# Kernel optimization log

Hardware: AMD Instinct MI355X
Metric: run time of the kernel (lower is better)

The kernel has to match this reference:

```python
import jax, jax.numpy as jnp
import numpy as np

TEMPERATURE = 0.07
EPS = 1e-12  # F.normalize eps


def setup_inputs() -> dict:
    key = jax.random.key(0)
    k1, k2, k3 = jax.random.split(key, 3)
    B, D, N_CLASSES = 4096, 256, 1000
    return {
        "z_i": jax.random.normal(k1, (B, D), dtype=jnp.float32),
        "z_j": jax.random.normal(k2, (B, D), dtype=jnp.float32),
        "labels": jax.random.randint(k3, (B,), 0, N_CLASSES, dtype=jnp.int64),
    }


def _l2_normalize(x):
    norm = jnp.sqrt(jnp.sum(x * x, axis=1, keepdims=True))
    return x / jnp.maximum(norm, EPS)


def reference(z_i, z_j, labels):
    zi = _l2_normalize(z_i)
    zj = _l2_normalize(z_j)
    z = jnp.concatenate([zi, zj], axis=0)          # (2B, D)
    lab = jnp.concatenate([labels, labels], axis=0)  # (2B,)
    N = z.shape[0]

    sim = jnp.matmul(z, z.T) / TEMPERATURE          # (2B, 2B)

    eye = jnp.eye(N, dtype=bool)
    same = lab[:, None] == lab[None, :]
    pos_mask = same & ~eye                          # positives: same label, not self
    neg_mask = ~same                                # negatives: different label

    # pos_sim_i = sum of similarities over positives (a sum, per original code)
    pos_sim = jnp.sum(jnp.where(pos_mask, sim, 0.0), axis=1)  # (2B,)
    # log(neg_sim_i) = logsumexp over negatives (stable, same math as sum of exp)
    lse_neg = jax.nn.logsumexp(jnp.where(neg_mask, sim, -jnp.inf), axis=1)
    # -log(exp(p) / (exp(p) + n)) = log(1 + exp(log n - p))
    loss_i = jnp.logaddexp(0.0, lse_neg - pos_sim)  # (2B,)

    has_pos = jnp.any(pos_mask, axis=1)
    loss = jnp.sum(jnp.where(has_pos, loss_i, 0.0)) / N
    return loss
```

## Files before the change

kernel.cpp:

```cpp
#include <hip/hip_runtime.h>

#define NROWS 8192
#define BQ    4096
#define DDIM  256
#define INV_T (1.0f/0.07f)
#define K2EXP (1.4426950408889634f/0.07f)

typedef short bf16x8 __attribute__((ext_vector_type(8)));
typedef float f32x4  __attribute__((ext_vector_type(4)));
typedef unsigned short u16;

__device__ __forceinline__ u16 f2bf(float f) {
  unsigned u = __float_as_uint(f);
  u += 0x7fffu + ((u >> 16) & 1u);
  return (u16)(u >> 16);
}

__global__ void norm_cast_kernel(const float* __restrict__ zi,
                                 const float* __restrict__ zj,
                                 u16* __restrict__ zb,
                                 float* __restrict__ partials) {
  int wave = threadIdx.x >> 6;
  int lane = threadIdx.x & 63;
  int row  = blockIdx.x * 4 + wave;
  const float* src = (row < BQ) ? (zi + (size_t)row * DDIM)
                                : (zj + (size_t)(row - BQ) * DDIM);
  float4 v = ((const float4*)src)[lane];
  float s = v.x*v.x + v.y*v.y + v.z*v.z + v.w*v.w;
  #pragma unroll
  for (int m = 32; m; m >>= 1) s += __shfl_xor(s, m, 64);
  float scale = 1.0f / fmaxf(sqrtf(s), 1e-12f);
  ushort4 o;
  o.x = f2bf(v.x * scale); o.y = f2bf(v.y * scale);
  o.z = f2bf(v.z * scale); o.w = f2bf(v.w * scale);
  ((ushort4*)(zb + (size_t)row * DDIM))[lane] = o;
  if (threadIdx.x < 128)
    partials[(size_t)blockIdx.x * 128 + threadIdx.x] = 0.0f;
}

#define GL2LDS(gp, lp) \
  __builtin_amdgcn_global_load_lds((__attribute__((address_space(1))) void*)(gp), \
                                   (__attribute__((address_space(3))) void*)(lp), 16, 0, 0)

__global__ __launch_bounds__(256) void simloss_kernel(
    const u16* __restrict__ zb, const int* __restrict__ labels,
    float* __restrict__ pos_p, float* __restrict__ neg_p) {
  __shared__ __align__(16) u16 lsA[128 * 32];
  __shared__ __align__(16) u16 lsB[128 * 32];

  const int tid  = threadIdx.x;
  const int w    = tid >> 6;
  const int lane = tid & 63;
  const int ln   = lane & 15;
  const int qd   = lane >> 4;
  const int wr   = w >> 1;
  const int wc   = w & 1;
  const int r0   = blockIdx.x * 128;
  const int cb   = blockIdx.y * 512;

  const int strow = lane >> 2;
  const int slot  = lane & 3;
  const int stk   = (slot ^ ((strow >> 1) & 3)) * 8;
  const int rdsw  = (ln >> 1) & 3;

  int rowidx[16], rowlab[16];
  #pragma unroll
  for (int ri = 0; ri < 4; ++ri)
    #pragma unroll
    for (int r = 0; r < 4; ++r) {
      int slt = ri * 4 + r;
      int row = r0 + wr * 64 + ri * 16 + qd * 4 + r;
      rowidx[slt] = row;
      rowlab[slt] = labels[row & (BQ - 1)];
    }

  float posA[16], negA[16];
  #pragma unroll
  for (int i = 0; i < 16; ++i) { posA[i] = 0.0f; negA[i] = 0.0f; }

  for (int ci = 0; ci < 4; ++ci) {
    const int c0 = cb + ci * 128;
    int colv[4], clab[4];
    #pragma unroll
    for (int mi = 0; mi < 4; ++mi) {
      colv[mi] = c0 + wc * 64 + mi * 16 + ln;
      clab[mi] = labels[colv[mi] & (BQ - 1)];
    }

    const f32x4 z4 = {0.f, 0.f, 0.f, 0.f};
    f32x4 acc[4][4];
    #pragma unroll
    for (int ri = 0; ri < 4; ++ri)
      #pragma unroll
      for (int mi = 0; mi < 4; ++mi) acc[ri][mi] = z4;

    for (int kk = 0; kk < 8; ++kk) {
      const int k0 = kk * 32;
      #pragma unroll
      for (int j = 0; j < 2; ++j) {
        int rbase = w * 32 + j * 16;
        const u16* ga = zb + (size_t)(r0 + rbase + strow) * DDIM + k0 + stk;
        GL2LDS(ga, &lsA[rbase * 32]);
        const u16* gb = zb + (size_t)(c0 + rbase + strow) * DDIM + k0 + stk;
        GL2LDS(gb, &lsB[rbase * 32]);
      }
      __syncthreads();

      bf16x8 av[4], bv[4];
      #pragma unroll
      for (int ri = 0; ri < 4; ++ri)
        av[ri] = *(const bf16x8*)&lsA[(wr * 64 + ri * 16 + ln) * 32 + (qd ^ rdsw) * 8];
      #pragma unroll
      for (int mi = 0; mi < 4; ++mi)
        bv[mi] = *(const bf16x8*)&lsB[(wc * 64 + mi * 16 + ln) * 32 + (qd ^ rdsw) * 8];
      #pragma unroll
      for (int ri = 0; ri < 4; ++ri)
        #pragma unroll
        for (int mi = 0; mi < 4; ++mi)
          acc[ri][mi] = __builtin_amdgcn_mfma_f32_16x16x32_bf16(
              av[ri], bv[mi], acc[ri][mi], 0, 0, 0);
      __syncthreads();
    }

    #pragma unroll
    for (int ri = 0; ri < 4; ++ri)
      #pragma unroll
      for (int mi = 0; mi < 4; ++mi) {
        f32x4 v = acc[ri][mi];
        #pragma unroll
        for (int r = 0; r < 4; ++r) {
          int slt = ri * 4 + r;
          float s = v[r];
          bool same = (rowlab[slt] == clab[mi]);
          bool diag = (rowidx[slt] == colv[mi]);
          posA[slt] += (same && !diag) ? s : 0.0f;
          negA[slt] += same ? 0.0f : __builtin_amdgcn_exp2f(s * K2EXP);
        }
      }
  }

  #pragma unroll
  for (int i = 0; i < 16; ++i) {
    #pragma unroll
    for (int m = 1; m < 16; m <<= 1) {
      posA[i] += __shfl_xor(posA[i], m, 64);
      negA[i] += __shfl_xor(negA[i], m, 64);
    }
  }
  if (ln == 0) {
    #pragma unroll
    for (int i = 0; i < 16; ++i) {
      atomicAdd(&pos_p[(size_t)blockIdx.y * NROWS + rowidx[i]], posA[i]);
      atomicAdd(&neg_p[(size_t)blockIdx.y * NROWS + rowidx[i]], negA[i]);
    }
  }
}

__global__ void loss_kernel(const float* __restrict__ pos_p,
                            const float* __restrict__ neg_p,
                            float* __restrict__ out) {
  int row = blockIdx.x * 256 + threadIdx.x;
  float p = 0.0f, n = 0.0f;
  #pragma unroll
  for (int s = 0; s < 16; ++s) {
    p += pos_p[(size_t)s * NROWS + row];
    n += neg_p[(size_t)s * NROWS + row];
  }
  float l = log1pf(expf(logf(n) - p * INV_T));
  #pragma unroll
  for (int m = 32; m; m >>= 1) l += __shfl_xor(l, m, 64);
  __shared__ float red[4];
  if ((threadIdx.x & 63) == 0) red[threadIdx.x >> 6] = l;
  __syncthreads();
  if (threadIdx.x == 0) {
    float tot = red[0] + red[1] + red[2] + red[3];
    atomicAdd(out, tot * (1.0f / NROWS));
  }
}

extern "C" void kernel_launch(void* const* d_in, const int* in_sizes, int n_in,
                              void* d_out, int out_size, void* d_ws, size_t ws_size,
                              hipStream_t stream) {
  const float* zi     = (const float*)d_in[0];
  const float* zj     = (const float*)d_in[1];
  const int*   labels = (const int*)d_in[2];
  float*       out    = (float*)d_out;

  char* w = (char*)d_ws;
  u16*   zb    = (u16*)w;
  float* pos_p = (float*)(w + (size_t)NROWS * DDIM * sizeof(u16));
  float* neg_p = pos_p + 16 * NROWS;

  hipMemsetAsync(out, 0, sizeof(float), stream);
  hipLaunchKernelGGL(norm_cast_kernel, dim3(2048), dim3(256), 0, stream,
                     zi, zj, zb, pos_p);
  hipLaunchKernelGGL(simloss_kernel, dim3(64, 16), dim3(256), 0, stream,
                     zb, labels, pos_p, neg_p);
  hipLaunchKernelGGL(loss_kernel, dim3(32), dim3(256), 0, stream,
                     pos_p, neg_p, out);
}
```

Baseline: 125.5 us.

## Exploit Gram-matrix symmetry by computing only lower-triangular tiles

The similarity kernel now launches one block per 128x128 tile in the lower triangle of the symmetric Gram matrix, instead of covering the full matrix. Each off-diagonal tile adds its results to both its rows and, through column reductions, to its columns. This roughly halves the matmul and exp work, at the cost of extra column reductions and more atomics landing on a single shared partial buffer. The loss kernel becomes a single 1024-thread block that writes the output directly, which also removes the memset launch.

```diff
diff --git a/kernel.cpp b/kernel.cpp
--- a/kernel.cpp
+++ b/kernel.cpp
@@ -5,6 +5,8 @@
 #define DDIM  256
 #define INV_T (1.0f/0.07f)
 #define K2EXP (1.4426950408889634f/0.07f)
+#define NTILE 64
+#define NBLK  (NTILE*(NTILE+1)/2)
 
 typedef short bf16x8 __attribute__((ext_vector_type(8)));
 typedef float f32x4  __attribute__((ext_vector_type(4)));
@@ -34,8 +36,8 @@
   o.x = f2bf(v.x * scale); o.y = f2bf(v.y * scale);
   o.z = f2bf(v.z * scale); o.w = f2bf(v.w * scale);
   ((ushort4*)(zb + (size_t)row * DDIM))[lane] = o;
-  if (threadIdx.x < 128)
-    partials[(size_t)blockIdx.x * 128 + threadIdx.x] = 0.0f;
+  if (threadIdx.x < 8)
+    partials[(size_t)blockIdx.x * 8 + threadIdx.x] = 0.0f;
 }
 
 #define GL2LDS(gp, lp) \
@@ -55,8 +57,15 @@
   const int qd   = lane >> 4;
   const int wr   = w >> 1;
   const int wc   = w & 1;
-  const int r0   = blockIdx.x * 128;
-  const int cb   = blockIdx.y * 512;
+
+  int bid = blockIdx.x;
+  int bx = (int)((sqrtf(8.0f * (float)bid + 1.0f) - 1.0f) * 0.5f);
+  while ((bx + 1) * (bx + 2) / 2 <= bid) ++bx;
+  while (bx * (bx + 1) / 2 > bid) --bx;
+  int by = bid - bx * (bx + 1) / 2;
+  const bool offdiag = (bx != by);
+  const int r0 = bx * 128;
+  const int c0 = by * 128;
 
   const int strow = lane >> 2;
   const int slot  = lane & 3;
@@ -73,71 +82,72 @@
       rowidx[slt] = row;
       rowlab[slt] = labels[row & (BQ - 1)];
     }
-
-  float posA[16], negA[16];
-  #pragma unroll
-  for (int i = 0; i < 16; ++i) { posA[i] = 0.0f; negA[i] = 0.0f; }
-
-  for (int ci = 0; ci < 4; ++ci) {
-    const int c0 = cb + ci * 128;
-    int colv[4], clab[4];
-    #pragma unroll
-    for (int mi = 0; mi < 4; ++mi) {
-      colv[mi] = c0 + wc * 64 + mi * 16 + ln;
-      clab[mi] = labels[colv[mi] & (BQ - 1)];
-    }
-
-    const f32x4 z4 = {0.f, 0.f, 0.f, 0.f};
-    f32x4 acc[4][4];
+  int colv[4], clab[4];
+  #pragma unroll
+  for (int mi = 0; mi < 4; ++mi) {
+    colv[mi] = c0 + wc * 64 + mi * 16 + ln;
+    clab[mi] = labels[colv[mi] & (BQ - 1)];
+  }
+
+  const f32x4 z4 = {0.f, 0.f, 0.f, 0.f};
+  f32x4 acc[4][4];
+  #pragma unroll
+  for (int ri = 0; ri < 4; ++ri)
+    #pragma unroll
+    for (int mi = 0; mi < 4; ++mi) acc[ri][mi] = z4;
+
+  for (int kk = 0; kk < 8; ++kk) {
+    const int k0 = kk * 32;
+    #pragma unroll
+    for (int j = 0; j < 2; ++j) {
+      int rbase = w * 32 + j * 16;
+      const u16* ga = zb + (size_t)(r0 + rbase + strow) * DDIM + k0 + stk;
+      GL2LDS(ga, &lsA[rbase * 32]);
+      const u16* gb = zb + (size_t)(c0 + rbase + strow) * DDIM + k0 + stk;
+      GL2LDS(gb, &lsB[rbase * 32]);
+    }
+    __syncthreads();
+
+    bf16x8 av[4], bv[4];
+    #pragma unroll
+    for (int ri = 0; ri < 4; ++ri)
+      av[ri] = *(const bf16x8*)&lsA[(wr * 64 + ri * 16 + ln) * 32 + (qd ^ rdsw) * 8];
+    #pragma unroll
+    for (int mi = 0; mi < 4; ++mi)
+      bv[mi] = *(const bf16x8*)&lsB[(wc * 64 + mi * 16 + ln) * 32 + (qd ^ rdsw) * 8];
     #pragma unroll
     for (int ri = 0; ri < 4; ++ri)
       #pragma unroll
-      for (int mi = 0; mi < 4; ++mi) acc[ri][mi] = z4;
-
-    for (int kk = 0; kk < 8; ++kk) {
-      const int k0 = kk * 32;
+      for (int mi = 0; mi < 4; ++mi)
+        acc[ri][mi] = __builtin_amdgcn_mfma_f32_16x16x32_bf16(
+            av[ri], bv[mi], acc[ri][mi], 0, 0, 0);
+    __syncthreads();
+  }
+
+  float posA[16], negA[16];
+  #pragma unroll
+  for (int i = 0; i < 16; ++i) { posA[i] = 0.0f; negA[i] = 0.0f; }
+  float colp[4], coln[4];
+  #pragma unroll
+  for (int i = 0; i < 4; ++i) { colp[i] = 0.0f; coln[i] = 0.0f; }
+
+  #pragma unroll
+  for (int ri = 0; ri < 4; ++ri)
+    #pragma unroll
+    for (int mi = 0; mi < 4; ++mi) {
+      f32x4 v = acc[ri][mi];
       #pragma unroll
-      for (int j = 0; j < 2; ++j) {
-        int rbase = w * 32 + j * 16;
-        const u16* ga = zb + (size_t)(r0 + rbase + strow) * DDIM + k0 + stk;
-        GL2LDS(ga, &lsA[rbase * 32]);
-        const u16* gb = zb + (size_t)(c0 + rbase + strow) * DDIM + k0 + stk;
-        GL2LDS(gb, &lsB[rbase * 32]);
+      for (int r = 0; r < 4; ++r) {
+        int slt = ri * 4 + r;
+        float s = v[r];
+        bool same = (rowlab[slt] == clab[mi]);
+        bool dg   = (rowidx[slt] == colv[mi]);
+        float pc = (same && !dg) ? s : 0.0f;
+        float nc = same ? 0.0f : __builtin_amdgcn_exp2f(s * K2EXP);
+        posA[slt] += pc;  negA[slt] += nc;
+        colp[mi]  += pc;  coln[mi]  += nc;
       }
-      __syncthreads();
-
-      bf16x8 av[4], bv[4];
-      #pragma unroll
-      for (int ri = 0; ri < 4; ++ri)
-        av[ri] = *(const bf16x8*)&lsA[(wr * 64 + ri * 16 + ln) * 32 + (qd ^ rdsw) * 8];
-      #pragma unroll
-      for (int mi = 0; mi < 4; ++mi)
-        bv[mi] = *(const bf16x8*)&lsB[(wc * 64 + mi * 16 + ln) * 32 + (qd ^ rdsw) * 8];
-      #pragma unroll
-      for (int ri = 0; ri < 4; ++ri)
-        #pragma unroll
-        for (int mi = 0; mi < 4; ++mi)
-          acc[ri][mi] = __builtin_amdgcn_mfma_f32_16x16x32_bf16(
-              av[ri], bv[mi], acc[ri][mi], 0, 0, 0);
-      __syncthreads();
-    }
-
-    #pragma unroll
-    for (int ri = 0; ri < 4; ++ri)
-      #pragma unroll
-      for (int mi = 0; mi < 4; ++mi) {
-        f32x4 v = acc[ri][mi];
-        #pragma unroll
-        for (int r = 0; r < 4; ++r) {
-          int slt = ri * 4 + r;
-          float s = v[r];
-          bool same = (rowlab[slt] == clab[mi]);
-          bool diag = (rowidx[slt] == colv[mi]);
-          posA[slt] += (same && !diag) ? s : 0.0f;
-          negA[slt] += same ? 0.0f : __builtin_amdgcn_exp2f(s * K2EXP);
-        }
-      }
-  }
+    }
 
   #pragma unroll
   for (int i = 0; i < 16; ++i) {
@@ -150,8 +160,25 @@
   if (ln == 0) {
     #pragma unroll
     for (int i = 0; i < 16; ++i) {
-      atomicAdd(&pos_p[(size_t)blockIdx.y * NROWS + rowidx[i]], posA[i]);
-      atomicAdd(&neg_p[(size_t)blockIdx.y * NROWS + rowidx[i]], negA[i]);
+      atomicAdd(&pos_p[rowidx[i]], posA[i]);
+      atomicAdd(&neg_p[rowidx[i]], negA[i]);
+    }
+  }
+
+  if (offdiag) {
+    #pragma unroll
+    for (int mi = 0; mi < 4; ++mi) {
+      colp[mi] += __shfl_xor(colp[mi], 16, 64);
+      colp[mi] += __shfl_xor(colp[mi], 32, 64);
+      coln[mi] += __shfl_xor(coln[mi], 16, 64);
+      coln[mi] += __shfl_xor(coln[mi], 32, 64);
+    }
+    if (qd == 0) {
+      #pragma unroll
+      for (int mi = 0; mi < 4; ++mi) {
+        atomicAdd(&pos_p[colv[mi]], colp[mi]);
+        atomicAdd(&neg_p[colv[mi]], coln[mi]);
+      }
     }
   }
 }
@@ -159,22 +186,25 @@
 __global__ void loss_kernel(const float* __restrict__ pos_p,
                             const float* __restrict__ neg_p,
                             float* __restrict__ out) {
-  int row = blockIdx.x * 256 + threadIdx.x;
-  float p = 0.0f, n = 0.0f;
-  #pragma unroll
-  for (int s = 0; s < 16; ++s) {
-    p += pos_p[(size_t)s * NROWS + row];
-    n += neg_p[(size_t)s * NROWS + row];
-  }
-  float l = log1pf(expf(logf(n) - p * INV_T));
-  #pragma unroll
-  for (int m = 32; m; m >>= 1) l += __shfl_xor(l, m, 64);
-  __shared__ float red[4];
-  if ((threadIdx.x & 63) == 0) red[threadIdx.x >> 6] = l;
+  int t = threadIdx.x;
+  float lsum = 0.0f;
+  #pragma unroll
+  for (int rr = 0; rr < 8; ++rr) {
+    int row = rr * 1024 + t;
+    float p = pos_p[row] * INV_T;
+    float n = neg_p[row];
+    lsum += log1pf(expf(logf(n) - p));
+  }
+  #pragma unroll
+  for (int m = 32; m; m >>= 1) lsum += __shfl_xor(lsum, m, 64);
+  __shared__ float red[16];
+  if ((t & 63) == 0) red[t >> 6] = lsum;
   __syncthreads();
-  if (threadIdx.x == 0) {
-    float tot = red[0] + red[1] + red[2] + red[3];
-    atomicAdd(out, tot * (1.0f / NROWS));
+  if (t == 0) {
+    float tot = 0.0f;
+    #pragma unroll
+    for (int i = 0; i < 16; ++i) tot += red[i];
+    out[0] = tot * (1.0f / NROWS);
   }
 }
 
@@ -189,13 +219,12 @@
   char* w = (char*)d_ws;
   u16*   zb    = (u16*)w;
   float* pos_p = (float*)(w + (size_t)NROWS * DDIM * sizeof(u16));
-  float* neg_p = pos_p + 16 * NROWS;
-
-  hipMemsetAsync(out, 0, sizeof(float), stream);
+  float* neg_p = pos_p + NROWS;
+
   hipLaunchKernelGGL(norm_cast_kernel, dim3(2048), dim3(256), 0, stream,
                      zi, zj, zb, pos_p);
-  hipLaunchKernelGGL(simloss_kernel, dim3(64, 16), dim3(256), 0, stream,
+  hipLaunchKernelGGL(simloss_kernel, dim3(NBLK), dim3(256), 0, stream,
                      zb, labels, pos_p, neg_p);
-  hipLaunchKernelGGL(loss_kernel, dim3(32), dim3(256), 0, stream,
+  hipLaunchKernelGGL(loss_kernel, dim3(1), dim3(1024), 0, stream,
                      pos_p, neg_p, out);
 }
```

New measurement: 213.5 us. +70.1%, slower.
